# Kernel optimization log

Hardware: AMD Instinct MI355X
Metric: run time of the kernel (lower is better)

The kernel has to match this reference:

```python
import jax, jax.numpy as jnp
import numpy as np

N_NODES = 100000
IN_CH, HID_CH, OUT_CH = 128, 128, 64
N_EDGES = 1600000


def gcn_conv(x, W, b, src, dst, num_nodes):
    """PyG GCNConv: x@W -> symmetric-normalized aggregation with self-loops -> +bias."""
    h = x @ W  # [N, out]
    loop = jnp.arange(num_nodes, dtype=src.dtype)
    src_a = jnp.concatenate([src, loop])  # add self-loops
    dst_a = jnp.concatenate([dst, loop])
    # degree of destination nodes over augmented edge set (edge_weight = 1)
    deg = jax.ops.segment_sum(jnp.ones_like(dst_a, dtype=h.dtype), dst_a,
                              num_segments=num_nodes)
    dis = jnp.where(deg > 0, jax.lax.rsqrt(jnp.maximum(deg, 1e-30)), 0.0)
    norm = dis[src_a] * dis[dst_a]  # [E+N]
    msg = h[src_a] * norm[:, None]  # gather + normalize
    out = jax.ops.segment_sum(msg, dst_a, num_segments=num_nodes)  # scatter-add
    return out + b


def setup_inputs() -> dict:
    key = jax.random.key(0)
    ks = jax.random.split(key, 9)
    x = jax.random.normal(ks[0], (N_NODES, IN_CH), dtype=jnp.float32)
    edge_index = jax.random.randint(ks[1], (2, N_EDGES), 0, N_NODES, dtype=jnp.int64)
    def glorot(k, fan_in, fan_out):
        s = np.sqrt(6.0 / (fan_in + fan_out)).astype(np.float32)
        return jax.random.uniform(k, (fan_in, fan_out), jnp.float32, -s, s)
    return {
        "x": x,
        "edge_index": edge_index,
        "W1": glorot(ks[2], IN_CH, HID_CH),
        "b1": jnp.zeros((HID_CH,), jnp.float32),
        "W2": glorot(ks[3], HID_CH, HID_CH),
        "b2": jnp.zeros((HID_CH,), jnp.float32),
        "Wo": glorot(ks[4], HID_CH, OUT_CH),
        "bo": jnp.zeros((OUT_CH,), jnp.float32),
    }


def reference(x, edge_index, W1, b1, W2, b2, Wo, bo):
    src, dst = edge_index[0], edge_index[1]
    n = x.shape[0]
    x1 = jax.nn.relu(gcn_conv(x, W1, b1, src, dst, n))
    x2 = jax.nn.relu(gcn_conv(x1, W2, b2, src, dst, n))
    return (x1 + x2) @ Wo + bo
```

## Files before the change

kernel.cpp:

```cpp
#include <hip/hip_runtime.h>
#include <hip/hip_fp16.h>

#define N_NODES 100000
#define N_EDGES 1600000
#define CH 128
#define OCH 64
#define NBUCKET 391
#define CAP 8192
#define BIN_CHUNK 4096
#define ZROW N_NODES

typedef _Float16 half8 __attribute__((ext_vector_type(8)));
typedef float f32x4 __attribute__((ext_vector_type(4)));

__device__ __forceinline__ ushort f2h(float f) {
    _Float16 h = (_Float16)f;
    return *(ushort*)&h;
}

__device__ __forceinline__ uint pkadd(uint a, uint b) {
    __half2 r = __hadd2(*(__half2*)&a, *(__half2*)&b);
    return *(uint*)&r;
}

__device__ __forceinline__ uint4 pk4(uint4 a, uint4 b) {
    a.x = pkadd(a.x, b.x); a.y = pkadd(a.y, b.y);
    a.z = pkadd(a.z, b.z); a.w = pkadd(a.w, b.w);
    return a;
}

__device__ __forceinline__ int swz(int row, int k) {
    return row * 128 + ((((k >> 3) ^ (row & 15)) << 3) | (k & 7));
}


__global__ __launch_bounds__(512) void k_bin(const int* __restrict__ src,
                                             const int* __restrict__ dst,
                                             int* __restrict__ bfill,
                                             int* __restrict__ bin) {
    __shared__ int hist[512];
    __shared__ int wbase[512];
    __shared__ int cur[512];
    const int t = threadIdx.x;
    const int e0 = blockIdx.x * BIN_CHUNK;

    hist[t] = 0;
    __syncthreads();

    int ss[8], bb[8], dl[8];
#pragma unroll
    for (int j = 0; j < 8; ++j) {
        int e = e0 + j * 512 + t;
        bb[j] = -1;
        if (e < N_EDGES) {
            int s = src[e], d = dst[e];
            ss[j] = s; dl[j] = d & 255; bb[j] = d >> 8;
            atomicAdd(&hist[bb[j]], 1);
        }
    }
    __syncthreads();

    int v = hist[t];
    for (int off = 1; off < 512; off <<= 1) {
        int tv = (t >= off) ? hist[t - off] : 0;
        __syncthreads();
        hist[t] += tv;
        __syncthreads();
    }
    int excl = hist[t] - v;
    if (t < NBUCKET && v > 0) {
        int gb = atomicAdd(&bfill[t], v);
        wbase[t] = gb - excl;
    }
    cur[t] = excl;
    __syncthreads();

#pragma unroll
    for (int j = 0; j < 8; ++j) {
        if (bb[j] >= 0) {
            int p = atomicAdd(&cur[bb[j]], 1);
            bin[bb[j] * CAP + wbase[bb[j]] + p] = (ss[j] << 8) | dl[j];
        }
    }
}

__global__ __launch_bounds__(512) void k_scan_prep(const int* __restrict__ bfill,
                                                   int* __restrict__ bbase,
                                                   const float* __restrict__ W1,
                                                   const float* __restrict__ W2,
                                                   const float* __restrict__ Wo,
                                                   ushort* __restrict__ W1s,
                                                   ushort* __restrict__ W2s,
                                                   ushort* __restrict__ WoTs,
                                                   ushort* __restrict__ h) {
    if (blockIdx.x == 0) {
        __shared__ int tmp[512];
        int t = threadIdx.x;
        int v = (t < NBUCKET) ? bfill[t] : 0;
        tmp[t] = v;
        __syncthreads();
        for (int off = 1; off < 512; off <<= 1) {
            int tv = (t >= off) ? tmp[t - off] : 0;
            __syncthreads();
            tmp[t] += tv;
            __syncthreads();
        }
        if (t < NBUCKET) bbase[t] = tmp[t] - v;
    } else if (blockIdx.x == 81) {
        if (threadIdx.x < CH) h[(size_t)ZROW * CH + threadIdx.x] = 0;
    } else {
        int i = (blockIdx.x - 1) * 512 + threadIdx.x;
        if (i < 16384) {
            int k = i >> 7, n = i & 127;
            W1s[swz(n, k)] = f2h(W1[i]);
        } else if (i < 32768) {
            int j = i - 16384, k = j >> 7, n = j & 127;
            W2s[swz(n, k)] = f2h(W2[j]);
        } else if (i < 40960) {
            int j = i - 32768, k = j >> 6, n = j & 63;
            WoTs[swz(n, k)] = f2h(Wo[j]);
        }
    }
}

__global__ __launch_bounds__(256) void k_build(const int* __restrict__ bfill,
                                               const int* __restrict__ bbase,
                                               const int* __restrict__ bin,
                                               int* __restrict__ esrc,
                                               int2* __restrict__ scnt,
                                               float* __restrict__ dis) {
    __shared__ int cnt_l[256];
    __shared__ int cur_l[256];
    __shared__ int sortbuf[CAP];
    const int t = threadIdx.x;
    const int b = blockIdx.x;
    const int n = bfill[b];
    const int base = bbase[b];
    const int* brec = bin + b * CAP;

    cnt_l[t] = 0;
    __syncthreads();
    for (int i = t; i < n; i += 256)
        atomicAdd(&cnt_l[brec[i] & 255], 1);
    __syncthreads();

    int v = cnt_l[t];
    for (int off = 1; off < 256; off <<= 1) {
        int tv = (t >= off) ? cnt_l[t - off] : 0;
        __syncthreads();
        cnt_l[t] += tv;
        __syncthreads();
    }
    int excl = cnt_l[t] - v;
    int node = b * 256 + t;
    if (node < N_NODES) {
        scnt[node] = make_int2(base + excl, v);
        dis[node] = rsqrtf((float)(v + 1));
    }
    cur_l[t] = excl;
    __syncthreads();

    for (int i = t; i < n; i += 256) {
        int rec = brec[i];
        int p = atomicAdd(&cur_l[rec & 255], 1);
        sortbuf[p] = rec >> 8;
    }
    __syncthreads();
    for (int i = t; i < n; i += 256)
        esrc[base + i] = sortbuf[i];
}


template <typename IT>
__global__ __launch_bounds__(512) void k_gemm_mfma(const IT* __restrict__ A,
                                                   const ushort* __restrict__ Ws,
                                                   const float* __restrict__ dis,
                                                   ushort* __restrict__ out) {
    __shared__ ushort sB[128 * 128];
    __shared__ ushort sA[128 * 136];
    const int tid = threadIdx.x;
    const int row0 = blockIdx.x * 128;

    for (int i = tid; i < 2048; i += 512)
        ((float4*)sB)[i] = ((const float4*)Ws)[i];

    for (int i = tid; i < 4096; i += 512) {
        int m = i >> 5, u = i & 31, k4 = u << 2;
        int r = row0 + m;
        ushort4 pk = make_ushort4(0, 0, 0, 0);
        if (r < N_NODES) {
            if constexpr (sizeof(IT) == 4) {
                float4 a = ((const float4*)A)[r * 32 + u];
                pk = make_ushort4(f2h(a.x), f2h(a.y), f2h(a.z), f2h(a.w));
            } else {
                pk = ((const ushort4*)A)[r * 32 + u];
            }
        }
        *(ushort4*)&sA[swz(m, k4)] = pk;
    }
    __syncthreads();

    const int lane = tid & 63, wv = tid >> 6;
    const int mrow = lane & 15, quad = lane >> 4;
    f32x4 acc[8] = {};
#pragma unroll
    for (int kc = 0; kc < 4; ++kc) {
        int g = kc * 4 + quad;
        half8 a = *(const half8*)&sA[(wv * 16 + mrow) * 128 + ((g ^ mrow) << 3)];
#pragma unroll
        for (int nt = 0; nt < 8; ++nt) {
            half8 b = *(const half8*)&sB[(nt * 16 + mrow) * 128 + ((g ^ mrow) << 3)];
            acc[nt] = __builtin_amdgcn_mfma_f32_16x16x32_f16(a, b, acc[nt], 0, 0, 0);
        }
    }

    const int rbase4 = wv * 16 + quad * 4;
    float ds[4];
#pragma unroll
    for (int rg = 0; rg < 4; ++rg)
        ds[rg] = (row0 + rbase4 + rg < N_NODES) ? dis[row0 + rbase4 + rg] : 0.f;

    __syncthreads();
#pragma unroll
    for (int nt = 0; nt < 8; ++nt) {
#pragma unroll
        for (int rg = 0; rg < 4; ++rg)
            sA[(rbase4 + rg) * 136 + nt * 16 + mrow] = f2h(acc[nt][rg] * ds[rg]);
    }
    __syncthreads();

#pragma unroll
    for (int k = 0; k < 4; ++k) {
        int idx = tid + k * 512;
        int m = idx >> 4, c16 = idx & 15;
        int r = row0 + m;
        if (r < N_NODES) {
            uint4 vv = *(const uint4*)&sA[m * 136 + c16 * 8];
            ((uint4*)out)[(size_t)r * 16 + c16] = vv;
        }
    }
}


struct Ictx { int n; int grp; int s0, s1, s2, s3, s4, s5; };
struct Gt { uint4 t0, t1, t2, t3, t4, t5, slf; };

__device__ __forceinline__ Ictx idx_stage(const int* __restrict__ esrc, int off, int n, int q) {
    Ictx c; c.n = n;
    const int* ep = esrc + off;
    int r0 = ep[q], r1 = ep[q + 4], r2 = ep[q + 8];
    int r3 = ep[q + 12], r4 = ep[q + 16], r5 = ep[q + 20];
    bool grp = (q + 12 < n);
    bool ok = (n <= q + 24);
    c.grp = grp;
    c.s0 = (grp || q < n)      ? r0 : ZROW;
    c.s1 = (grp || q + 4 < n)  ? r1 : ZROW;
    c.s2 = (grp || q + 8 < n)  ? r2 : ZROW;
    c.s3 = grp                 ? r3 : ZROW;
    c.s4 = (grp && ok && q + 16 < n) ? r4 : ZROW;
    c.s5 = (grp && ok && q + 20 < n) ? r5 : ZROW;
    return c;
}

__device__ __forceinline__ Gt gather_stage(const Ictx& c, int v, int l,
                                           const uint4* __restrict__ h16) {
    Gt g;
    g.t0 = h16[(size_t)c.s0 * 16 + l];
    g.t1 = h16[(size_t)c.s1 * 16 + l];
    g.t2 = h16[(size_t)c.s2 * 16 + l];
    g.t3 = h16[(size_t)c.s3 * 16 + l];
    g.t4 = h16[(size_t)c.s4 * 16 + l];
    g.t5 = h16[(size_t)c.s5 * 16 + l];
    g.slf = h16[(size_t)v * 16 + l];
    return g;
}

__device__ __forceinline__ void acc_finish(const Gt& g, const Ictx& c, int v, int q, int l,
                                           const int* __restrict__ esrc, int off,
                                           const uint4* __restrict__ h16,
                                           float dsv, float4 b0, float4 b1,
                                           ushort* __restrict__ out) {
    uint4 aA = make_uint4(0, 0, 0, 0), aB = make_uint4(0, 0, 0, 0);
    aA = pk4(aA, g.t0);
    if (c.grp) aB = pk4(aB, g.t1); else aA = pk4(aA, g.t1);
    aA = pk4(aA, g.t2);
    if (c.grp) aB = pk4(aB, g.t3); else aA = pk4(aA, g.t3);
    aA = pk4(aA, g.t4);
    aA = pk4(aA, g.t5);
    if (c.n > q + 24) {
        const int* ep = esrc + off;
        int i = q + 16;
        for (; i + 12 < c.n; i += 16) {
            uint4 u0 = h16[(size_t)ep[i] * 16 + l];
            uint4 u1 = h16[(size_t)ep[i + 4] * 16 + l];
            uint4 u2 = h16[(size_t)ep[i + 8] * 16 + l];
            uint4 u3 = h16[(size_t)ep[i + 12] * 16 + l];
            aA = pk4(aA, u0); aB = pk4(aB, u1); aA = pk4(aA, u2); aB = pk4(aB, u3);
        }
        for (; i < c.n; i += 4) aA = pk4(aA, h16[(size_t)ep[i] * 16 + l]);
    }
    aA = pk4(aA, aB);
    aA.x = pkadd(aA.x, (uint)__shfl_xor((int)aA.x, 16));
    aA.y = pkadd(aA.y, (uint)__shfl_xor((int)aA.y, 16));
    aA.z = pkadd(aA.z, (uint)__shfl_xor((int)aA.z, 16));
    aA.w = pkadd(aA.w, (uint)__shfl_xor((int)aA.w, 16));
    aA.x = pkadd(aA.x, (uint)__shfl_xor((int)aA.x, 32));
    aA.y = pkadd(aA.y, (uint)__shfl_xor((int)aA.y, 32));
    aA.z = pkadd(aA.z, (uint)__shfl_xor((int)aA.z, 32));
    aA.w = pkadd(aA.w, (uint)__shfl_xor((int)aA.w, 32));

    if (q == 0) {
        aA = pk4(aA, g.slf);
        float2 a0 = __half22float2(*(__half2*)&aA.x);
        float2 a1 = __half22float2(*(__half2*)&aA.y);
        float2 a2 = __half22float2(*(__half2*)&aA.z);
        float2 a3 = __half22float2(*(__half2*)&aA.w);
        a0.x = fmaxf(a0.x * dsv + b0.x, 0.f); a0.y = fmaxf(a0.y * dsv + b0.y, 0.f);
        a1.x = fmaxf(a1.x * dsv + b0.z, 0.f); a1.y = fmaxf(a1.y * dsv + b0.w, 0.f);
        a2.x = fmaxf(a2.x * dsv + b1.x, 0.f); a2.y = fmaxf(a2.y * dsv + b1.y, 0.f);
        a3.x = fmaxf(a3.x * dsv + b1.z, 0.f); a3.y = fmaxf(a3.y * dsv + b1.w, 0.f);
        __half2 o0 = __float22half2_rn(a0);
        __half2 o1 = __float22half2_rn(a1);
        __half2 o2 = __float22half2_rn(a2);
        __half2 o3 = __float22half2_rn(a3);
        ((uint4*)out)[v * 16 + l] =
            make_uint4(*(uint*)&o0, *(uint*)&o1, *(uint*)&o2, *(uint*)&o3);
    }
}

__global__ __launch_bounds__(256) void k_agg(const int2* __restrict__ scnt,
                                             const int* __restrict__ esrc,
                                             const ushort* __restrict__ h,
                                             const float* __restrict__ dis,
                                             const float* __restrict__ bias,
                                             ushort* __restrict__ out) {
    const int w = threadIdx.x >> 6;
    const int vb = blockIdx.x * 16 + w * 4;
    const int lane = threadIdx.x & 63, q = lane >> 4, l = lane & 15;
    const uint4* h16 = (const uint4*)h;

    int2 m0 = scnt[vb], m1 = scnt[vb + 1], m2 = scnt[vb + 2], m3 = scnt[vb + 3];
    float d0 = dis[vb], d1 = dis[vb + 1], d2 = dis[vb + 2], d3 = dis[vb + 3];
    float4 b0 = ((const float4*)bias)[2 * l];
    float4 b1 = ((const float4*)bias)[2 * l + 1];

    Ictx c0 = idx_stage(esrc, m0.x, m0.y, q);
    Gt g0 = gather_stage(c0, vb, l, h16);
    Ictx c1 = idx_stage(esrc, m1.x, m1.y, q);
    Gt g1 = gather_stage(c1, vb + 1, l, h16);
    Ictx c2 = idx_stage(esrc, m2.x, m2.y, q);
    acc_finish(g0, c0, vb, q, l, esrc, m0.x, h16, d0, b0, b1, out);
    Gt g2 = gather_stage(c2, vb + 2, l, h16);
    Ictx c3 = idx_stage(esrc, m3.x, m3.y, q);
    acc_finish(g1, c1, vb + 1, q, l, esrc, m1.x, h16, d1, b0, b1, out);
    Gt g3 = gather_stage(c3, vb + 3, l, h16);
    acc_finish(g2, c2, vb + 2, q, l, esrc, m2.x, h16, d2, b0, b1, out);
    acc_finish(g3, c3, vb + 3, q, l, esrc, m3.x, h16, d3, b0, b1, out);
}


__global__ __launch_bounds__(512) void k_final_mfma(const ushort* __restrict__ x1,
                                                    const ushort* __restrict__ x2,
                                                    const ushort* __restrict__ Ws,
                                                    const float* __restrict__ bo,
                                                    float* __restrict__ out) {
    __shared__ ushort sB[64 * 128];
    __shared__ float sF[128 * 68];
    ushort* sA = (ushort*)sF;
    const int tid = threadIdx.x;
    const int row0 = blockIdx.x * 128;

    for (int i = tid; i < 1024; i += 512)
        ((float4*)sB)[i] = ((const float4*)Ws)[i];

    for (int i = tid; i < 4096; i += 512) {
        int m = i >> 5, u = i & 31, k4 = u << 2;
        int r = row0 + m;
        uint2 pk = make_uint2(0, 0);
        if (r < N_NODES) {
            uint2 ua = ((const uint2*)x1)[r * 32 + u];
            uint2 ub = ((const uint2*)x2)[r * 32 + u];
            __half2 s0 = __hadd2(*(__half2*)&ua.x, *(__half2*)&ub.x);
            __half2 s1 = __hadd2(*(__half2*)&ua.y, *(__half2*)&ub.y);
            pk = make_uint2(*(uint*)&s0, *(uint*)&s1);
        }
        *(uint2*)&sA[swz(m, k4)] = pk;
    }
    __syncthreads();

    const int lane = tid & 63, wv = tid >> 6;
    const int mrow = lane & 15, quad = lane >> 4;
    f32x4 acc[4] = {};
#pragma unroll
    for (int kc = 0; kc < 4; ++kc) {
        int g = kc * 4 + quad;
        half8 a = *(const half8*)&sA[(wv * 16 + mrow) * 128 + ((g ^ mrow) << 3)];
#pragma unroll
        for (int nt = 0; nt < 4; ++nt) {
            half8 b = *(const half8*)&sB[(nt * 16 + mrow) * 128 + ((g ^ mrow) << 3)];
            acc[nt] = __builtin_amdgcn_mfma_f32_16x16x32_f16(a, b, acc[nt], 0, 0, 0);
        }
    }

    const int rbase4 = wv * 16 + quad * 4;
    __syncthreads();
#pragma unroll
    for (int nt = 0; nt < 4; ++nt) {
        float bb = bo[nt * 16 + mrow];
#pragma unroll
        for (int rg = 0; rg < 4; ++rg)
            sF[(rbase4 + rg) * 68 + nt * 16 + mrow] = acc[nt][rg] + bb;
    }
    __syncthreads();

#pragma unroll
    for (int k = 0; k < 4; ++k) {
        int idx = tid + k * 512;
        int m = idx >> 4, c16 = idx & 15;
        int r = row0 + m;
        if (r < N_NODES) {
            uint4 vv = *(const uint4*)&sF[m * 68 + c16 * 4];
            ((uint4*)out)[(size_t)r * 16 + c16] = vv;
        }
    }
}


extern "C" void kernel_launch(void* const* d_in, const int* in_sizes, int n_in,
                              void* d_out, int out_size, void* d_ws, size_t ws_size,
                              hipStream_t stream) {
    const float* x  = (const float*)d_in[0];
    const int*   ei = (const int*)d_in[1];
    const int*   src = ei;
    const int*   dst = ei + N_EDGES;
    const float* W1 = (const float*)d_in[2];
    const float* b1 = (const float*)d_in[3];
    const float* W2 = (const float*)d_in[4];
    const float* b2 = (const float*)d_in[5];
    const float* Wo = (const float*)d_in[6];
    const float* bo = (const float*)d_in[7];
    float* out = (float*)d_out;

    char* ws = (char*)d_ws;
    int*    bfill  = (int*)ws;            ws += 2048;
    int*    bbase  = (int*)ws;            ws += 2048;
    int2*   scnt   = (int2*)ws;           ws += 800000;
    float*  dis    = (float*)ws;          ws += 400000;
    int*    bin    = (int*)ws;            ws += (size_t)NBUCKET * CAP * 4;
    int*    esrc   = (int*)ws;            ws += (size_t)N_EDGES * 4;
    ushort* W1s    = (ushort*)ws;         ws += 32768;
    ushort* W2s    = (ushort*)ws;         ws += 32768;
    ushort* WoTs   = (ushort*)ws;         ws += 16384;
    ushort* h      = (ushort*)ws;         ws += (size_t)(N_NODES + 1) * CH * 2;
    ushort* x1     = (ushort*)ws;         ws += (size_t)N_NODES * CH * 2;
    ushort* x2     = (ushort*)ws;

    const int gG = (N_NODES + 127) / 128;
    const int gA = N_NODES / 16;

    hipMemsetAsync(bfill, 0, 2048, stream);
    k_bin<<<(N_EDGES + BIN_CHUNK - 1) / BIN_CHUNK, 512, 0, stream>>>(src, dst, bfill, bin);
    k_scan_prep<<<82, 512, 0, stream>>>(bfill, bbase, W1, W2, Wo, W1s, W2s, WoTs, h);
    k_build<<<NBUCKET, 256, 0, stream>>>(bfill, bbase, bin, esrc, scnt, dis);

    k_gemm_mfma<float><<<gG, 512, 0, stream>>>(x, W1s, dis, h);
    k_agg<<<gA, 256, 0, stream>>>(scnt, esrc, h, dis, b1, x1);

    k_gemm_mfma<ushort><<<gG, 512, 0, stream>>>(x1, W2s, dis, h);
    k_agg<<<gA, 256, 0, stream>>>(scnt, esrc, h, dis, b2, x2);

    k_final_mfma<<<gG, 512, 0, stream>>>(x1, x2, WoTs, bo, out);
}
```

Before: 309.0 us.

## Compute degrees with global atomics and co-schedule edge binning with first GEMM

Node degrees are now counted up front with global atomics in the prep kernel, so the first GEMM no longer waits on the CSR build to get normalization. Edge binning blocks and first-layer GEMM blocks are merged into one launch, letting the two independent jobs overlap. The bucket prefix scan moves into k_build, which now uses 512 threads, and rsqrt is recomputed from deg wherever needed instead of reading a dis array. This trades heavy global atomic contention on deg and a larger shared footprint for the binning blocks against fewer serialized launches.

Result: slower. 364.6 us (+18.0%).

```diff
diff --git a/kernel.cpp b/kernel.cpp
--- a/kernel.cpp
+++ b/kernel.cpp
@@ -9,6 +9,7 @@
 #define CAP 8192
 #define BIN_CHUNK 4096
 #define ZROW N_NODES
+#define GG 782
 
 typedef _Float16 half8 __attribute__((ext_vector_type(8)));
 typedef float f32x4 __attribute__((ext_vector_type(4)));
@@ -34,152 +35,45 @@
 }
 
 
-__global__ __launch_bounds__(512) void k_bin(const int* __restrict__ src,
-                                             const int* __restrict__ dst,
-                                             int* __restrict__ bfill,
-                                             int* __restrict__ bin) {
-    __shared__ int hist[512];
-    __shared__ int wbase[512];
-    __shared__ int cur[512];
-    const int t = threadIdx.x;
-    const int e0 = blockIdx.x * BIN_CHUNK;
-
-    hist[t] = 0;
-    __syncthreads();
-
-    int ss[8], bb[8], dl[8];
-#pragma unroll
-    for (int j = 0; j < 8; ++j) {
-        int e = e0 + j * 512 + t;
-        bb[j] = -1;
-        if (e < N_EDGES) {
-            int s = src[e], d = dst[e];
-            ss[j] = s; dl[j] = d & 255; bb[j] = d >> 8;
-            atomicAdd(&hist[bb[j]], 1);
-        }
-    }
-    __syncthreads();
-
-    int v = hist[t];
-    for (int off = 1; off < 512; off <<= 1) {
-        int tv = (t >= off) ? hist[t - off] : 0;
-        __syncthreads();
-        hist[t] += tv;
-        __syncthreads();
-    }
-    int excl = hist[t] - v;
-    if (t < NBUCKET && v > 0) {
-        int gb = atomicAdd(&bfill[t], v);
-        wbase[t] = gb - excl;
-    }
-    cur[t] = excl;
-    __syncthreads();
-
-#pragma unroll
-    for (int j = 0; j < 8; ++j) {
-        if (bb[j] >= 0) {
-            int p = atomicAdd(&cur[bb[j]], 1);
-            bin[bb[j] * CAP + wbase[bb[j]] + p] = (ss[j] << 8) | dl[j];
-        }
-    }
-}
-
-__global__ __launch_bounds__(512) void k_scan_prep(const int* __restrict__ bfill,
-                                                   int* __restrict__ bbase,
-                                                   const float* __restrict__ W1,
-                                                   const float* __restrict__ W2,
-                                                   const float* __restrict__ Wo,
-                                                   ushort* __restrict__ W1s,
-                                                   ushort* __restrict__ W2s,
-                                                   ushort* __restrict__ WoTs,
-                                                   ushort* __restrict__ h) {
-    if (blockIdx.x == 0) {
-        __shared__ int tmp[512];
-        int t = threadIdx.x;
-        int v = (t < NBUCKET) ? bfill[t] : 0;
-        tmp[t] = v;
-        __syncthreads();
-        for (int off = 1; off < 512; off <<= 1) {
-            int tv = (t >= off) ? tmp[t - off] : 0;
-            __syncthreads();
-            tmp[t] += tv;
-            __syncthreads();
-        }
-        if (t < NBUCKET) bbase[t] = tmp[t] - v;
-    } else if (blockIdx.x == 81) {
-        if (threadIdx.x < CH) h[(size_t)ZROW * CH + threadIdx.x] = 0;
-    } else {
-        int i = (blockIdx.x - 1) * 512 + threadIdx.x;
+__global__ __launch_bounds__(512) void k_prep(const float* __restrict__ W1,
+                                              const float* __restrict__ W2,
+                                              const float* __restrict__ Wo,
+                                              ushort* __restrict__ W1s,
+                                              ushort* __restrict__ W2s,
+                                              ushort* __restrict__ WoTs,
+                                              ushort* __restrict__ h,
+                                              const int* __restrict__ dst,
+                                              int* __restrict__ deg) {
+    const int b = blockIdx.x, t = threadIdx.x;
+    if (b < 80) {
+        int i = b * 512 + t;
         if (i < 16384) {
             int k = i >> 7, n = i & 127;
             W1s[swz(n, k)] = f2h(W1[i]);
         } else if (i < 32768) {
             int j = i - 16384, k = j >> 7, n = j & 127;
             W2s[swz(n, k)] = f2h(W2[j]);
-        } else if (i < 40960) {
+        } else {
             int j = i - 32768, k = j >> 6, n = j & 63;
             WoTs[swz(n, k)] = f2h(Wo[j]);
         }
-    }
-}
-
-__global__ __launch_bounds__(256) void k_build(const int* __restrict__ bfill,
-                                               const int* __restrict__ bbase,
-                                               const int* __restrict__ bin,
-                                               int* __restrict__ esrc,
-                                               int2* __restrict__ scnt,
-                                               float* __restrict__ dis) {
-    __shared__ int cnt_l[256];
-    __shared__ int cur_l[256];
-    __shared__ int sortbuf[CAP];
-    const int t = threadIdx.x;
-    const int b = blockIdx.x;
-    const int n = bfill[b];
-    const int base = bbase[b];
-    const int* brec = bin + b * CAP;
-
-    cnt_l[t] = 0;
-    __syncthreads();
-    for (int i = t; i < n; i += 256)
-        atomicAdd(&cnt_l[brec[i] & 255], 1);
-    __syncthreads();
-
-    int v = cnt_l[t];
-    for (int off = 1; off < 256; off <<= 1) {
-        int tv = (t >= off) ? cnt_l[t - off] : 0;
-        __syncthreads();
-        cnt_l[t] += tv;
-        __syncthreads();
-    }
-    int excl = cnt_l[t] - v;
-    int node = b * 256 + t;
-    if (node < N_NODES) {
-        scnt[node] = make_int2(base + excl, v);
-        dis[node] = rsqrtf((float)(v + 1));
-    }
-    cur_l[t] = excl;
-    __syncthreads();
-
-    for (int i = t; i < n; i += 256) {
-        int rec = brec[i];
-        int p = atomicAdd(&cur_l[rec & 255], 1);
-        sortbuf[p] = rec >> 8;
-    }
-    __syncthreads();
-    for (int i = t; i < n; i += 256)
-        esrc[base + i] = sortbuf[i];
+    } else if (b == 80) {
+        if (t < CH) h[(size_t)ZROW * CH + t] = 0;
+    } else {
+        int e = (b - 81) * 512 + t;
+        atomicAdd(&deg[dst[e]], 1);
+    }
 }
 
 
 template <typename IT>
-__global__ __launch_bounds__(512) void k_gemm_mfma(const IT* __restrict__ A,
-                                                   const ushort* __restrict__ Ws,
-                                                   const float* __restrict__ dis,
-                                                   ushort* __restrict__ out) {
-    __shared__ ushort sB[128 * 128];
-    __shared__ ushort sA[128 * 136];
+__device__ __forceinline__ void gemm_block(int bidx, const IT* __restrict__ A,
+                                           const ushort* __restrict__ Ws,
+                                           const int* __restrict__ deg,
+                                           ushort* __restrict__ out,
+                                           ushort* sB, ushort* sA) {
     const int tid = threadIdx.x;
-    const int row0 = blockIdx.x * 128;
+    const int row0 = bidx * 128;
 
     for (int i = tid; i < 2048; i += 512)
         ((float4*)sB)[i] = ((const float4*)Ws)[i];
@@ -217,8 +111,10 @@
     const int rbase4 = wv * 16 + quad * 4;
     float ds[4];
 #pragma unroll
-    for (int rg = 0; rg < 4; ++rg)
-        ds[rg] = (row0 + rbase4 + rg < N_NODES) ? dis[row0 + rbase4 + rg] : 0.f;
+    for (int rg = 0; rg < 4; ++rg) {
+        int r = row0 + rbase4 + rg;
+        ds[rg] = (r < N_NODES) ? rsqrtf((float)(deg[r] + 1)) : 0.f;
+    }
 
     __syncthreads();
 #pragma unroll
@@ -239,6 +135,131 @@
             ((uint4*)out)[(size_t)r * 16 + c16] = vv;
         }
     }
+}
+
+
+__global__ __launch_bounds__(512) void k_bin_gemm(const int* __restrict__ src,
+                                                  const int* __restrict__ dst,
+                                                  int* __restrict__ bfill,
+                                                  int* __restrict__ bin,
+                                                  const float* __restrict__ A,
+                                                  const ushort* __restrict__ Ws,
+                                                  const int* __restrict__ deg,
+                                                  ushort* __restrict__ out) {
+    __shared__ __align__(16) char smem[32768 + 34816];
+    if (blockIdx.x < NBUCKET) {
+        int* hist  = (int*)smem;
+        int* wbase = (int*)(smem + 2048);
+        int* cur   = (int*)(smem + 4096);
+        const int t = threadIdx.x;
+        const int e0 = blockIdx.x * BIN_CHUNK;
+
+        hist[t] = 0;
+        __syncthreads();
+
+        int ss[8], bb[8], dl[8];
+#pragma unroll
+        for (int j = 0; j < 8; ++j) {
+            int e = e0 + j * 512 + t;
+            bb[j] = -1;
+            if (e < N_EDGES) {
+                int s = src[e], d = dst[e];
+                ss[j] = s; dl[j] = d & 255; bb[j] = d >> 8;
+                atomicAdd(&hist[bb[j]], 1);
+            }
+        }
+        __syncthreads();
+
+        int v = hist[t];
+        for (int off = 1; off < 512; off <<= 1) {
+            int tv = (t >= off) ? hist[t - off] : 0;
+            __syncthreads();
+            hist[t] += tv;
+            __syncthreads();
+        }
+        int excl = hist[t] - v;
+        if (t < NBUCKET && v > 0) {
+            int gb = atomicAdd(&bfill[t], v);
+            wbase[t] = gb - excl;
+        }
+        cur[t] = excl;
+        __syncthreads();
+
+#pragma unroll
+        for (int j = 0; j < 8; ++j) {
+            if (bb[j] >= 0) {
+                int p = atomicAdd(&cur[bb[j]], 1);
+                bin[bb[j] * CAP + wbase[bb[j]] + p] = (ss[j] << 8) | dl[j];
+            }
+        }
+    } else {
+        gemm_block<float>(blockIdx.x - NBUCKET, A, Ws, deg, out,
+                          (ushort*)smem, (ushort*)(smem + 32768));
+    }
+}
+
+
+template <typename IT>
+__global__ __launch_bounds__(512) void k_gemm_mfma(const IT* __restrict__ A,
+                                                   const ushort* __restrict__ Ws,
+                                                   const int* __restrict__ deg,
+                                                   ushort* __restrict__ out) {
+    __shared__ __align__(16) char smem[32768 + 34816];
+    gemm_block<IT>(blockIdx.x, A, Ws, deg, out, (ushort*)smem, (ushort*)(smem + 32768));
+}
+
+
+__global__ __launch_bounds__(512) void k_build(const int* __restrict__ bfill,
+                                               const int* __restrict__ bin,
+                                               int* __restrict__ esrc,
+                                               int2* __restrict__ scnt) {
+    __shared__ int pre[512];
+    __shared__ int cnt_l[256];
+    __shared__ int cur_l[256];
+    __shared__ int sortbuf[CAP];
+    const int t = threadIdx.x;
+    const int b = blockIdx.x;
+
+    pre[t] = (t < NBUCKET) ? bfill[t] : 0;
+    if (t < 256) cnt_l[t] = 0;
+    __syncthreads();
+    for (int off = 1; off < 512; off <<= 1) {
+        int tv = (t >= off) ? pre[t - off] : 0;
+        __syncthreads();
+        pre[t] += tv;
+        __syncthreads();
+    }
+    const int n = bfill[b];
+    const int base = pre[b] - n;
+    const int* brec = bin + b * CAP;
+
+    for (int i = t; i < n; i += 512)
+        atomicAdd(&cnt_l[brec[i] & 255], 1);
+    __syncthreads();
+
+    int v = (t < 256) ? cnt_l[t] : 0;
+    for (int off = 1; off < 256; off <<= 1) {
+        int tv = (t >= off && t < 256) ? cnt_l[t - off] : 0;
+        __syncthreads();
+        if (t < 256) cnt_l[t] += tv;
+        __syncthreads();
+    }
+    if (t < 256) {
+        int excl = cnt_l[t] - v;
+        int node = b * 256 + t;
+        if (node < N_NODES) scnt[node] = make_int2(base + excl, v);
+        cur_l[t] = excl;
+    }
+    __syncthreads();
+
+    for (int i = t; i < n; i += 512) {
+        int rec = brec[i];
+        int p = atomicAdd(&cur_l[rec & 255], 1);
+        sortbuf[p] = rec >> 8;
+    }
+    __syncthreads();
+    for (int i = t; i < n; i += 512)
+        esrc[base + i] = sortbuf[i];
 }
 
 
@@ -331,7 +352,7 @@
 __global__ __launch_bounds__(256) void k_agg(const int2* __restrict__ scnt,
                                              const int* __restrict__ esrc,
                                              const ushort* __restrict__ h,
-                                             const float* __restrict__ dis,
+                                             const int* __restrict__ deg,
                                              const float* __restrict__ bias,
                                              ushort* __restrict__ out) {
     const int w = threadIdx.x >> 6;
@@ -340,7 +361,10 @@
     const uint4* h16 = (const uint4*)h;
 
     int2 m0 = scnt[vb], m1 = scnt[vb + 1], m2 = scnt[vb + 2], m3 = scnt[vb + 3];
-    float d0 = dis[vb], d1 = dis[vb + 1], d2 = dis[vb + 2], d3 = dis[vb + 3];
+    float d0 = rsqrtf((float)(deg[vb] + 1));
+    float d1 = rsqrtf((float)(deg[vb + 1] + 1));
+    float d2 = rsqrtf((float)(deg[vb + 2] + 1));
+    float d3 = rsqrtf((float)(deg[vb + 3] + 1));
     float4 b0 = ((const float4*)bias)[2 * l];
     float4 b1 = ((const float4*)bias)[2 * l + 1];
 
@@ -443,9 +467,8 @@
 
     char* ws = (char*)d_ws;
     int*    bfill  = (int*)ws;            ws += 2048;
-    int*    bbase  = (int*)ws;            ws += 2048;
+    int*    deg    = (int*)ws;            ws += 400000;
     int2*   scnt   = (int2*)ws;           ws += 800000;
-    float*  dis    = (float*)ws;          ws += 400000;
     int*    bin    = (int*)ws;            ws += (size_t)NBUCKET * CAP * 4;
     int*    esrc   = (int*)ws;            ws += (size_t)N_EDGES * 4;
     ushort* W1s    = (ushort*)ws;         ws += 32768;
@@ -455,19 +478,17 @@
     ushort* x1     = (ushort*)ws;         ws += (size_t)N_NODES * CH * 2;
     ushort* x2     = (ushort*)ws;
 
-    const int gG = (N_NODES + 127) / 128;
     const int gA = N_NODES / 16;
 
-    hipMemsetAsync(bfill, 0, 2048, stream);
-    k_bin<<<(N_EDGES + BIN_CHUNK - 1) / BIN_CHUNK, 512, 0, stream>>>(src, dst, bfill, bin);
-    k_scan_prep<<<82, 512, 0, stream>>>(bfill, bbase, W1, W2, Wo, W1s, W2s, WoTs, h);
-    k_build<<<NBUCKET, 256, 0, stream>>>(bfill, bbase, bin, esrc, scnt, dis);
-
-    k_gemm_mfma<float><<<gG, 512, 0, stream>>>(x, W1s, dis, h);
-    k_agg<<<gA, 256, 0, stream>>>(scnt, esrc, h, dis, b1, x1);
-
-    k_gemm_mfma<ushort><<<gG, 512, 0, stream>>>(x1, W2s, dis, h);
-    k_agg<<<gA, 256, 0, stream>>>(scnt, esrc, h, dis, b2, x2);
-
-    k_final_mfma<<<gG, 512, 0, stream>>>(x1, x2, WoTs, bo, out);
-}
+    hipMemsetAsync(bfill, 0, 2048 + 400000, stream);
+    k_prep<<<81 + 3125, 512, 0, stream>>>(W1, W2, Wo, W1s, W2s, WoTs, h, dst, deg);
+    k_bin_gemm<<<NBUCKET + GG, 512, 0, stream>>>(src, dst, bfill, bin, x, W1s, deg, h);
+    k_build<<<NBUCKET, 512, 0, stream>>>(bfill, bin, esrc, scnt);
+
+    k_agg<<<gA, 256, 0, stream>>>(scnt, esrc, h, deg, b1, x1);
+
+    k_gemm_mfma<ushort><<<GG, 512, 0, stream>>>(x1, W2s, deg, h);
+    k_agg<<<gA, 256, 0, stream>>>(scnt, esrc, h, deg, b2, x2);
+
+    k_final_mfma<<<GG, 512, 0, stream>>>(x1, x2, WoTs, bo, out);
+}
```

## Fuse weight prep into binning, stage bins in LDS, fold bucket scan into build

Applied to the files above, without the earlier changes.

Weight conversion and zero-row init move into the binning kernel as extra blocks. The separate bucket-prefix-scan kernel is removed: each build block now recomputes the prefix over bucket fills itself. Binning first sorts each chunk's records into shared memory by bucket, then writes them out contiguously, so the global stores to bin are less scattered. Build blocks widen to 512 threads. The aim is one fewer launch and better store coalescing, at the cost of a redundant scan in every build block and more shared memory.

New measurement: 297.7 us. 1.04x faster.

```diff
diff --git a/kernel.cpp b/kernel.cpp
--- a/kernel.cpp
+++ b/kernel.cpp
@@ -9,6 +9,7 @@
 #define CAP 8192
 #define BIN_CHUNK 4096
 #define ZROW N_NODES
+#define GG 782
 
 typedef _Float16 half8 __attribute__((ext_vector_type(8)));
 typedef float f32x4 __attribute__((ext_vector_type(4)));
@@ -34,16 +35,46 @@
 }
 
 
-__global__ __launch_bounds__(512) void k_bin(const int* __restrict__ src,
-                                             const int* __restrict__ dst,
-                                             int* __restrict__ bfill,
-                                             int* __restrict__ bin) {
+__global__ __launch_bounds__(512) void k_bin_prep(const int* __restrict__ src,
+                                                  const int* __restrict__ dst,
+                                                  int* __restrict__ bfill,
+                                                  int* __restrict__ bin,
+                                                  const float* __restrict__ W1,
+                                                  const float* __restrict__ W2,
+                                                  const float* __restrict__ Wo,
+                                                  ushort* __restrict__ W1s,
+                                                  ushort* __restrict__ W2s,
+                                                  ushort* __restrict__ WoTs,
+                                                  ushort* __restrict__ h) {
     __shared__ int hist[512];
+    __shared__ int excl[512];
     __shared__ int wbase[512];
     __shared__ int cur[512];
+    __shared__ int sbuf[BIN_CHUNK];
+    __shared__ ushort sbkt[BIN_CHUNK];
     const int t = threadIdx.x;
+
+    if (blockIdx.x >= NBUCKET) {
+        int b = blockIdx.x - NBUCKET;
+        if (b == 80) {
+            if (t < CH) h[(size_t)ZROW * CH + t] = 0;
+        } else {
+            int i = b * 512 + t;
+            if (i < 16384) {
+                int k = i >> 7, n = i & 127;
+                W1s[swz(n, k)] = f2h(W1[i]);
+            } else if (i < 32768) {
+                int j = i - 16384, k = j >> 7, n = j & 127;
+                W2s[swz(n, k)] = f2h(W2[j]);
+            } else {
+                int j = i - 32768, k = j >> 6, n = j & 63;
+                WoTs[swz(n, k)] = f2h(Wo[j]);
+            }
+        }
+        return;
+    }
+
     const int e0 = blockIdx.x * BIN_CHUNK;
-
     hist[t] = 0;
     __syncthreads();
 
@@ -67,106 +98,84 @@
         hist[t] += tv;
         __syncthreads();
     }
-    int excl = hist[t] - v;
-    if (t < NBUCKET && v > 0) {
-        int gb = atomicAdd(&bfill[t], v);
-        wbase[t] = gb - excl;
-    }
-    cur[t] = excl;
+    int ex = hist[t] - v;
+    excl[t] = ex;
+    cur[t] = ex;
+    if (t < NBUCKET && v > 0) wbase[t] = atomicAdd(&bfill[t], v);
     __syncthreads();
 
 #pragma unroll
     for (int j = 0; j < 8; ++j) {
         if (bb[j] >= 0) {
             int p = atomicAdd(&cur[bb[j]], 1);
-            bin[bb[j] * CAP + wbase[bb[j]] + p] = (ss[j] << 8) | dl[j];
-        }
-    }
-}
-
-__global__ __launch_bounds__(512) void k_scan_prep(const int* __restrict__ bfill,
-                                                   int* __restrict__ bbase,
-                                                   const float* __restrict__ W1,
-                                                   const float* __restrict__ W2,
-                                                   const float* __restrict__ Wo,
-                                                   ushort* __restrict__ W1s,
-                                                   ushort* __restrict__ W2s,
-                                                   ushort* __restrict__ WoTs,
-                                                   ushort* __restrict__ h) {
-    if (blockIdx.x == 0) {
-        __shared__ int tmp[512];
-        int t = threadIdx.x;
-        int v = (t < NBUCKET) ? bfill[t] : 0;
-        tmp[t] = v;
-        __syncthreads();
-        for (int off = 1; off < 512; off <<= 1) {
-            int tv = (t >= off) ? tmp[t - off] : 0;
-            __syncthreads();
-            tmp[t] += tv;
-            __syncthreads();
-        }
-        if (t < NBUCKET) bbase[t] = tmp[t] - v;
-    } else if (blockIdx.x == 81) {
-        if (threadIdx.x < CH) h[(size_t)ZROW * CH + threadIdx.x] = 0;
-    } else {
-        int i = (blockIdx.x - 1) * 512 + threadIdx.x;
-        if (i < 16384) {
-            int k = i >> 7, n = i & 127;
-            W1s[swz(n, k)] = f2h(W1[i]);
-        } else if (i < 32768) {
-            int j = i - 16384, k = j >> 7, n = j & 127;
-            W2s[swz(n, k)] = f2h(W2[j]);
-        } else if (i < 40960) {
-            int j = i - 32768, k = j >> 6, n = j & 63;
-            WoTs[swz(n, k)] = f2h(Wo[j]);
-        }
-    }
-}
-
-__global__ __launch_bounds__(256) void k_build(const int* __restrict__ bfill,
-                                               const int* __restrict__ bbase,
+            sbuf[p] = (ss[j] << 8) | dl[j];
+            sbkt[p] = (ushort)bb[j];
+        }
+    }
+    const int nloc = hist[511];
+    __syncthreads();
+
+    for (int i = t; i < nloc; i += 512) {
+        int b = sbkt[i];
+        bin[b * CAP + wbase[b] + (i - excl[b])] = sbuf[i];
+    }
+}
+
+
+__global__ __launch_bounds__(512) void k_build(const int* __restrict__ bfill,
                                                const int* __restrict__ bin,
                                                int* __restrict__ esrc,
                                                int2* __restrict__ scnt,
                                                float* __restrict__ dis) {
+    __shared__ int pre[512];
     __shared__ int cnt_l[256];
     __shared__ int cur_l[256];
     __shared__ int sortbuf[CAP];
     const int t = threadIdx.x;
     const int b = blockIdx.x;
+
+    pre[t] = (t < NBUCKET) ? bfill[t] : 0;
+    if (t < 256) cnt_l[t] = 0;
+    __syncthreads();
+    for (int off = 1; off < 512; off <<= 1) {
+        int tv = (t >= off) ? pre[t - off] : 0;
+        __syncthreads();
+        pre[t] += tv;
+        __syncthreads();
+    }
     const int n = bfill[b];
-    const int base = bbase[b];
+    const int base = pre[b] - n;
     const int* brec = bin + b * CAP;
 
-    cnt_l[t] = 0;
-    __syncthreads();
-    for (int i = t; i < n; i += 256)
+    for (int i = t; i < n; i += 512)
         atomicAdd(&cnt_l[brec[i] & 255], 1);
     __syncthreads();
 
-    int v = cnt_l[t];
+    int v = (t < 256) ? cnt_l[t] : 0;
     for (int off = 1; off < 256; off <<= 1) {
-        int tv = (t >= off) ? cnt_l[t - off] : 0;
-        __syncthreads();
-        cnt_l[t] += tv;
-        __syncthreads();
-    }
-    int excl = cnt_l[t] - v;
-    int node = b * 256 + t;
-    if (node < N_NODES) {
-        scnt[node] = make_int2(base + excl, v);
-        dis[node] = rsqrtf((float)(v + 1));
-    }
-    cur_l[t] = excl;
-    __syncthreads();
-
-    for (int i = t; i < n; i += 256) {
+        int tv = (t >= off && t < 256) ? cnt_l[t - off] : 0;
+        __syncthreads();
+        if (t < 256) cnt_l[t] += tv;
+        __syncthreads();
+    }
+    if (t < 256) {
+        int excl = cnt_l[t] - v;
+        int node = b * 256 + t;
+        if (node < N_NODES) {
+            scnt[node] = make_int2(base + excl, v);
+            dis[node] = rsqrtf((float)(v + 1));
+        }
+        cur_l[t] = excl;
+    }
+    __syncthreads();
+
+    for (int i = t; i < n; i += 512) {
         int rec = brec[i];
         int p = atomicAdd(&cur_l[rec & 255], 1);
         sortbuf[p] = rec >> 8;
     }
     __syncthreads();
-    for (int i = t; i < n; i += 256)
+    for (int i = t; i < n; i += 512)
         esrc[base + i] = sortbuf[i];
 }
 
@@ -217,8 +226,10 @@
     const int rbase4 = wv * 16 + quad * 4;
     float ds[4];
 #pragma unroll
-    for (int rg = 0; rg < 4; ++rg)
-        ds[rg] = (row0 + rbase4 + rg < N_NODES) ? dis[row0 + rbase4 + rg] : 0.f;
+    for (int rg = 0; rg < 4; ++rg) {
+        int r = row0 + rbase4 + rg;
+        ds[rg] = (r < N_NODES) ? dis[r] : 0.f;
+    }
 
     __syncthreads();
 #pragma unroll
@@ -443,7 +454,6 @@
 
     char* ws = (char*)d_ws;
     int*    bfill  = (int*)ws;            ws += 2048;
-    int*    bbase  = (int*)ws;            ws += 2048;
     int2*   scnt   = (int2*)ws;           ws += 800000;
     float*  dis    = (float*)ws;          ws += 400000;
     int*    bin    = (int*)ws;            ws += (size_t)NBUCKET * CAP * 4;
@@ -455,19 +465,18 @@
     ushort* x1     = (ushort*)ws;         ws += (size_t)N_NODES * CH * 2;
     ushort* x2     = (ushort*)ws;
 
-    const int gG = (N_NODES + 127) / 128;
     const int gA = N_NODES / 16;
 
     hipMemsetAsync(bfill, 0, 2048, stream);
-    k_bin<<<(N_EDGES + BIN_CHUNK - 1) / BIN_CHUNK, 512, 0, stream>>>(src, dst, bfill, bin);
-    k_scan_prep<<<82, 512, 0, stream>>>(bfill, bbase, W1, W2, Wo, W1s, W2s, WoTs, h);
-    k_build<<<NBUCKET, 256, 0, stream>>>(bfill, bbase, bin, esrc, scnt, dis);
-
-    k_gemm_mfma<float><<<gG, 512, 0, stream>>>(x, W1s, dis, h);
+    k_bin_prep<<<NBUCKET + 81, 512, 0, stream>>>(src, dst, bfill, bin,
+                                                 W1, W2, Wo, W1s, W2s, WoTs, h);
+    k_build<<<NBUCKET, 512, 0, stream>>>(bfill, bin, esrc, scnt, dis);
+
+    k_gemm_mfma<float><<<GG, 512, 0, stream>>>(x, W1s, dis, h);
     k_agg<<<gA, 256, 0, stream>>>(scnt, esrc, h, dis, b1, x1);
 
-    k_gemm_mfma<ushort><<<gG, 512, 0, stream>>>(x1, W2s, dis, h);
+    k_gemm_mfma<ushort><<<GG, 512, 0, stream>>>(x1, W2s, dis, h);
     k_agg<<<gA, 256, 0, stream>>>(scnt, esrc, h, dis, b2, x2);
 
-    k_final_mfma<<<gG, 512, 0, stream>>>(x1, x2, WoTs, bo, out);
-}
+    k_final_mfma<<<GG, 512, 0, stream>>>(x1, x2, WoTs, bo, out);
+}
```
